# Kernel tuning notes

Hardware: AMD Instinct MI355X
Metric: run time of the kernel (lower is better)

Reference implementation:

```python
import jax, jax.numpy as jnp
import numpy as np

B, T, QD, KD, AD = 64, 2048, 512, 512, 512
SCALING = 1.0
NEG = -1e10


def setup_inputs() -> dict:
    key = jax.random.key(0)
    ks = jax.random.split(key, 10)
    s = 0.02
    return {
        "query": jax.random.normal(ks[0], (B, QD), jnp.float32),
        "keys": jax.random.normal(ks[1], (B, T, KD), jnp.float32),
        "value": jax.random.normal(ks[2], (B, T, KD), jnp.float32),
        "cover": jax.random.uniform(ks[3], (B, T), jnp.float32),
        "key_len": jax.random.randint(ks[4], (B,), T // 2, T + 1),
        "Wq": jax.random.normal(ks[5], (QD, AD), jnp.float32) * s,
        "bq": jnp.zeros((AD,), jnp.float32),
        "Wk": jax.random.normal(ks[6], (KD, AD), jnp.float32) * s,
        "Wc": jax.random.normal(ks[7], (1, AD), jnp.float32) * s,
        "Wo": jax.random.normal(ks[8], (AD, 1), jnp.float32) * s,
    }


def reference(query, keys, value, cover, key_len, Wq, bq, Wk, Wc, Wo):
    # projections
    q = query @ Wq + bq                      # [B, A]
    k = jnp.einsum("btd,da->bta", keys, Wk)  # [B, T, A]
    c = cover[..., None] * Wc[0]             # [B, T, A]  (Linear(1, A), no bias)
    # additive energy
    e = jnp.tanh(q[:, None, :] + k + c)      # [B, T, A]
    energy = jnp.einsum("bta,ao->bot", e, Wo)  # [B, 1, T]
    # mask padded positions (t >= key_len)
    mask = jnp.arange(T)[None, None, :] >= key_len[:, None, None]  # [B, 1, T]
    energy = jnp.where(mask, NEG, energy)
    attn = jax.nn.softmax(energy * SCALING, axis=2)  # [B, 1, T]
    context = jnp.einsum("bqt,btd->bqd", attn, value)[:, 0, :]  # [B, KD]
    return context, attn
```

## Files before the change

### kernel.cpp

```cpp
#include <hip/hip_runtime.h>
#include <hip/hip_bf16.h>

#define B_ 64
#define T_ 2048
#define D_ 512
#define A_ 512
#define BM 128
#define BN 128
#define BK 32
#define NSTEP (D_/BK)

typedef float f32x4_t __attribute__((ext_vector_type(4)));
typedef short bf16x8_t __attribute__((ext_vector_type(8)));

#define GLL16(g, l) __builtin_amdgcn_global_load_lds( \
    (const __attribute__((address_space(1))) void*)(g), \
    (__attribute__((address_space(3))) void*)(l), 16, 0, 0)

__device__ __forceinline__ uint2 pack8u(float4 v0, float4 v1) {
  union { __hip_bfloat162 h[2]; uint2 u; } r;
  r.h[0] = __float22bfloat162_rn(make_float2(v0.x, v0.y));
  r.h[1] = __float22bfloat162_rn(make_float2(v0.z, v0.w));
  uint2 lo = r.u;
  r.h[0] = __float22bfloat162_rn(make_float2(v1.x, v1.y));
  r.h[1] = __float22bfloat162_rn(make_float2(v1.z, v1.w));
  return make_uint2(lo.x, lo.y), r.u;
}

__global__ void __launch_bounds__(256) qproj_kernel(
    const float* __restrict__ query, const float* __restrict__ Wq,
    const float* __restrict__ bq, float* __restrict__ qbuf) {
  __shared__ float qs[D_];
  const int b = blockIdx.x, tid = threadIdx.x;
  qs[tid] = query[b*D_ + tid];
  qs[tid+256] = query[b*D_ + tid + 256];
  __syncthreads();
  float a0 = bq[tid], a1 = bq[tid+256];
  for (int d = 0; d < D_; ++d) {
    const float qv = qs[d];
    a0 += qv * Wq[d*A_ + tid];
    a1 += qv * Wq[d*A_ + tid + 256];
  }
  qbuf[b*A_ + tid] = a0;
  qbuf[b*A_ + tid+256] = a1;
}

__global__ void __launch_bounds__(256) wkprep_kernel(
    const float* __restrict__ Wk, unsigned int* __restrict__ slab) {
  __shared__ float tile[32][65];
  const int kb = blockIdx.x >> 3;
  const int a0 = (blockIdx.x & 7) * 64;
  const int tid = threadIdx.x;
  for (int p = 0; p < 8; ++p) {
    const int idx = p*256 + tid;
    const int k = idx >> 6, al = idx & 63;
    tile[k][al] = Wk[(kb*32 + k)*A_ + a0 + al];
  }
  __syncthreads();
  const int al = tid >> 2, c = tid & 3;
  const int a = a0 + al;
  union { __hip_bfloat162 h[2]; uint2 u; } w0, w1;
  w0.h[0] = __float22bfloat162_rn(make_float2(tile[c*8+0][al], tile[c*8+1][al]));
  w0.h[1] = __float22bfloat162_rn(make_float2(tile[c*8+2][al], tile[c*8+3][al]));
  w1.h[0] = __float22bfloat162_rn(make_float2(tile[c*8+4][al], tile[c*8+5][al]));
  w1.h[1] = __float22bfloat162_rn(make_float2(tile[c*8+6][al], tile[c*8+7][al]));
  const int cpos = c ^ ((a >> 1) & 3);
  *(uint4*)(slab + (kb*512 + a)*16 + cpos*4) =
      make_uint4(w0.u.x, w0.u.y, w1.u.x, w1.u.y);
}

__global__ void __launch_bounds__(256, 4) energy_kernel(
    const float* __restrict__ keys, const float* __restrict__ cover,
    const int* __restrict__ key_len, const unsigned char* __restrict__ slab,
    const float* __restrict__ qbuf, const float* __restrict__ Wc,
    const float* __restrict__ Wo, float* __restrict__ epart) {
  __shared__ __align__(16) unsigned char Abuf[2][BM*64];
  __shared__ __align__(16) unsigned char Bbuf[2][BN*64];
  __shared__ float redbuf[4][64];

  const int d = blockIdx.x;
  const int logical = (d & 7) * 512 + (d >> 3);
  const int ct = logical & 3;
  const int tt = (logical >> 2) & 15;
  const int b  = logical >> 6;

  const int t0 = tt * BM;
  const int kl = key_len[b];
  if (t0 >= kl) return;

  const int tid = threadIdx.x;
  const int wid = tid >> 6;
  const int lane = tid & 63;
  const int lq = lane >> 4, lr = lane & 15;
  const int wm = wid >> 1, wn = wid & 1;

  const int arow = tid >> 1, ahalf = tid & 1;
  const float* aptr = keys + ((size_t)b * T_ + t0 + arow) * D_ + ahalf * 16;
  const int as = (arow >> 1) & 3;
  const int ad0 = arow*64 + (((ahalf*2+0) ^ as) << 4);
  const int ad1 = arow*64 + (((ahalf*2+1) ^ as) << 4);

  const unsigned char* bsl = slab + ct * 8192 + wid * 1024 + lane * 16;

  f32x4_t acc[4][4];
  #pragma unroll
  for (int i = 0; i < 4; ++i)
    #pragma unroll
    for (int j = 0; j < 4; ++j) acc[i][j] = 0.0f;

  int a_off[4], b_off[4];
  #pragma unroll
  for (int mf = 0; mf < 4; ++mf) {
    const int r = wm*64 + mf*16 + lr;
    a_off[mf] = r*64 + ((lq ^ ((r >> 1) & 3)) << 4);
  }
  #pragma unroll
  for (int nf = 0; nf < 4; ++nf) {
    const int r = wn*64 + nf*16 + lr;
    b_off[nf] = r*64 + ((lq ^ ((r >> 1) & 3)) << 4);
  }

  {
    const float4 v0 = *(const float4*)(aptr);
    const float4 v1 = *(const float4*)(aptr + 4);
    const float4 v2 = *(const float4*)(aptr + 8);
    const float4 v3 = *(const float4*)(aptr + 12);
    union { __hip_bfloat162 h[2]; uint2 u; } p0, p1, p2, p3;
    p0.h[0] = __float22bfloat162_rn(make_float2(v0.x, v0.y));
    p0.h[1] = __float22bfloat162_rn(make_float2(v0.z, v0.w));
    p1.h[0] = __float22bfloat162_rn(make_float2(v1.x, v1.y));
    p1.h[1] = __float22bfloat162_rn(make_float2(v1.z, v1.w));
    p2.h[0] = __float22bfloat162_rn(make_float2(v2.x, v2.y));
    p2.h[1] = __float22bfloat162_rn(make_float2(v2.z, v2.w));
    p3.h[0] = __float22bfloat162_rn(make_float2(v3.x, v3.y));
    p3.h[1] = __float22bfloat162_rn(make_float2(v3.z, v3.w));
    *(uint4*)(&Abuf[0][ad0]) = make_uint4(p0.u.x, p0.u.y, p1.u.x, p1.u.y);
    *(uint4*)(&Abuf[0][ad1]) = make_uint4(p2.u.x, p2.u.y, p3.u.x, p3.u.y);
    GLL16(bsl,        &Bbuf[0][wid*1024]);
    GLL16(bsl + 4096, &Bbuf[0][4096 + wid*1024]);
  }
  __syncthreads();

  for (int ks = 0; ks < NSTEP; ++ks) {
    const int cur = ks & 1;
    const bool pre = (ks + 1 < NSTEP);
    float4 v0, v1, v2, v3;
    if (pre) {
      const float* p = aptr + (ks + 1) * BK;
      v0 = *(const float4*)(p);
      v1 = *(const float4*)(p + 4);
      v2 = *(const float4*)(p + 8);
      v3 = *(const float4*)(p + 12);
      const unsigned char* g = bsl + (size_t)(ks+1)*32768;
      GLL16(g,        &Bbuf[cur^1][wid*1024]);
      GLL16(g + 4096, &Bbuf[cur^1][4096 + wid*1024]);
    }
    bf16x8_t aF[4], bF[4];
    #pragma unroll
    for (int mf = 0; mf < 4; ++mf) aF[mf] = *(const bf16x8_t*)(&Abuf[cur][a_off[mf]]);
    #pragma unroll
    for (int nf = 0; nf < 4; ++nf) bF[nf] = *(const bf16x8_t*)(&Bbuf[cur][b_off[nf]]);
    #pragma unroll
    for (int mf = 0; mf < 4; ++mf)
      #pragma unroll
      for (int nf = 0; nf < 4; ++nf)
        acc[mf][nf] = __builtin_amdgcn_mfma_f32_16x16x32_bf16(aF[mf], bF[nf], acc[mf][nf], 0, 0, 0);
    if (pre) {
      union { __hip_bfloat162 h[2]; uint2 u; } p0, p1, p2, p3;
      p0.h[0] = __float22bfloat162_rn(make_float2(v0.x, v0.y));
      p0.h[1] = __float22bfloat162_rn(make_float2(v0.z, v0.w));
      p1.h[0] = __float22bfloat162_rn(make_float2(v1.x, v1.y));
      p1.h[1] = __float22bfloat162_rn(make_float2(v1.z, v1.w));
      p2.h[0] = __float22bfloat162_rn(make_float2(v2.x, v2.y));
      p2.h[1] = __float22bfloat162_rn(make_float2(v2.z, v2.w));
      p3.h[0] = __float22bfloat162_rn(make_float2(v3.x, v3.y));
      p3.h[1] = __float22bfloat162_rn(make_float2(v3.z, v3.w));
      *(uint4*)(&Abuf[cur^1][ad0]) = make_uint4(p0.u.x, p0.u.y, p1.u.x, p1.u.y);
      *(uint4*)(&Abuf[cur^1][ad1]) = make_uint4(p2.u.x, p2.u.y, p3.u.x, p3.u.y);
    }
    __syncthreads();
  }

  float cov[4][4];
  #pragma unroll
  for (int mf = 0; mf < 4; ++mf)
    #pragma unroll
    for (int j = 0; j < 4; ++j)
      cov[mf][j] = cover[(size_t)b*T_ + t0 + wm*64 + mf*16 + lq*4 + j];

  float ep[4][4];
  #pragma unroll
  for (int mf = 0; mf < 4; ++mf)
    #pragma unroll
    for (int j = 0; j < 4; ++j) ep[mf][j] = 0.f;

  #pragma unroll
  for (int nf = 0; nf < 4; ++nf) {
    const int n = ct*BN + wn*64 + nf*16 + lr;
    const float qv = qbuf[b*A_ + n];
    const float wc = Wc[n];
    const float wo = Wo[n];
    #pragma unroll
    for (int mf = 0; mf < 4; ++mf)
      #pragma unroll
      for (int j = 0; j < 4; ++j) {
        float p = acc[mf][nf][j] + qv + cov[mf][j] * wc;
        p = fminf(fmaxf(p, -15.f), 15.f);
        const float t2 = __expf(2.f * p);
        ep[mf][j] += wo * ((t2 - 1.f) * __builtin_amdgcn_rcpf(t2 + 1.f));
      }
  }
  #pragma unroll
  for (int mf = 0; mf < 4; ++mf)
    #pragma unroll
    for (int j = 0; j < 4; ++j) {
      float v = ep[mf][j];
      v += __shfl_xor(v, 1); v += __shfl_xor(v, 2);
      v += __shfl_xor(v, 4); v += __shfl_xor(v, 8);
      ep[mf][j] = v;
    }
  if (lr == 0) {
    #pragma unroll
    for (int mf = 0; mf < 4; ++mf)
      #pragma unroll
      for (int j = 0; j < 4; ++j)
        redbuf[wid][mf*16 + lq*4 + j] = ep[mf][j];
  }
  __syncthreads();
  if (tid < BM) {
    const int wmm = tid >> 6, rl = tid & 63;
    epart[((size_t)ct*B_ + b)*T_ + t0 + tid] = redbuf[wmm*2][rl] + redbuf[wmm*2+1][rl];
  }
}

__global__ void __launch_bounds__(1024) softmax_kernel(
    const float* __restrict__ epart, const int* __restrict__ key_len,
    float* __restrict__ attn) {
  __shared__ float sredM[16];
  __shared__ float sredS[16];
  const int b = blockIdx.x, tid = threadIdx.x;
  const int kl = key_len[b];
  float e0 = -3.0e38f, e1 = -3.0e38f;
  if (tid < kl)
    e0 = epart[(size_t)b*T_ + tid] + epart[((size_t)B_ + b)*T_ + tid]
       + epart[((size_t)2*B_ + b)*T_ + tid] + epart[((size_t)3*B_ + b)*T_ + tid];
  if (tid + 1024 < kl)
    e1 = epart[(size_t)b*T_ + tid+1024] + epart[((size_t)B_ + b)*T_ + tid+1024]
       + epart[((size_t)2*B_ + b)*T_ + tid+1024] + epart[((size_t)3*B_ + b)*T_ + tid+1024];
  float m = fmaxf(e0, e1);
  for (int s = 32; s; s >>= 1) m = fmaxf(m, __shfl_xor(m, s));
  if ((tid & 63) == 0) sredM[tid >> 6] = m;
  __syncthreads();
  float M = -3.0e38f;
  #pragma unroll
  for (int i = 0; i < 16; ++i) M = fmaxf(M, sredM[i]);
  const float p0 = (tid < kl) ? __expf(e0 - M) : 0.f;
  const float p1 = (tid + 1024 < kl) ? __expf(e1 - M) : 0.f;
  float s = p0 + p1;
  for (int k = 32; k; k >>= 1) s += __shfl_xor(s, k);
  if ((tid & 63) == 0) sredS[tid >> 6] = s;
  __syncthreads();
  float S = 0.f;
  #pragma unroll
  for (int i = 0; i < 16; ++i) S += sredS[i];
  const float inv = 1.f / S;
  attn[b*T_ + tid] = p0 * inv;
  attn[b*T_ + tid + 1024] = p1 * inv;
}

__global__ void __launch_bounds__(256) ctxpart_kernel(
    const float* __restrict__ value, const float* __restrict__ attn,
    const int* __restrict__ key_len, float* __restrict__ partial) {
  __shared__ float att_s[256];
  const int b = blockIdx.y, ch = blockIdx.x;
  const int tid = threadIdx.x;
  const int kl = key_len[b];
  const int tstart = ch * 256;
  const int tend = min(256, kl - tstart);
  float ax = 0.f, ay = 0.f;
  if (tend > 0) {
    att_s[tid] = attn[b*T_ + tstart + tid];
    __syncthreads();
    const float2* vp = (const float2*)(value + ((size_t)b*T_ + tstart)*D_) + tid;
    #pragma unroll 4
    for (int i = 0; i < tend; ++i) {
      const float w = att_s[i];
      const float2 v = vp[(size_t)i * 256];
      ax += w * v.x; ay += w * v.y;
    }
  }
  float2* pp = (float2*)(partial + (size_t)(b*8 + ch)*D_) + tid;
  *pp = make_float2(ax, ay);
}

__global__ void __launch_bounds__(256) ctxsum_kernel(
    const float* __restrict__ partial, float* __restrict__ ctx) {
  const int b = blockIdx.x, tid = threadIdx.x;
  float sx = 0.f, sy = 0.f;
  #pragma unroll
  for (int c = 0; c < 8; ++c) {
    const float2 v = *((const float2*)(partial + (size_t)(b*8 + c)*D_) + tid);
    sx += v.x; sy += v.y;
  }
  *((float2*)(ctx + (size_t)b*D_) + tid) = make_float2(sx, sy);
}

extern "C" void kernel_launch(void* const* d_in, const int* in_sizes, int n_in,
                              void* d_out, int out_size, void* d_ws, size_t ws_size,
                              hipStream_t stream) {
  const float* query  = (const float*)d_in[0];
  const float* keys   = (const float*)d_in[1];
  const float* value  = (const float*)d_in[2];
  const float* cover  = (const float*)d_in[3];
  const int*   key_len= (const int*)d_in[4];
  const float* Wq     = (const float*)d_in[5];
  const float* bq     = (const float*)d_in[6];
  const float* Wk     = (const float*)d_in[7];
  const float* Wc     = (const float*)d_in[8];
  const float* Wo     = (const float*)d_in[9];

  float* out = (float*)d_out;
  float* ctx_out  = out;
  float* attn_out = out + B_*A_;

  float* ws = (float*)d_ws;
  float* qbuf    = ws;
  float* epart   = ws + 32768;
  float* partial = ws + 32768 + 524288;
  unsigned int* slab = (unsigned int*)(ws + 32768 + 524288 + 262144);

  qproj_kernel<<<B_, 256, 0, stream>>>(query, Wq, bq, qbuf);
  wkprep_kernel<<<128, 256, 0, stream>>>(Wk, slab);
  energy_kernel<<<B_*(T_/BM)*(A_/BN), 256, 0, stream>>>(
      keys, cover, key_len, (const unsigned char*)slab, qbuf, Wc, Wo, epart);
  softmax_kernel<<<B_, 1024, 0, stream>>>(epart, key_len, attn_out);
  ctxpart_kernel<<<dim3(8, B_), 256, 0, stream>>>(value, attn_out, key_len, partial);
  ctxsum_kernel<<<B_, 256, 0, stream>>>(partial, ctx_out);
}
```

Baseline: 224.6 us.

## Stream fp32 keys into LDS via global_load_lds and convert to bf16 at fragment load

The keys tile is now copied asynchronously into shared memory as fp32 with direct global-to-LDS loads, using an XOR-swizzled layout, instead of being loaded into registers and converted to bf16 before the LDS store. The bf16 conversion moves to the point where each wave reads its MFMA A fragments. This frees registers and takes the conversion and LDS store off the prefetch path, but it doubles the LDS footprint for A and makes every wave convert redundantly. Launch bounds occupancy is lowered from 4 to 3 to match.

```diff
diff --git a/kernel.cpp b/kernel.cpp
--- a/kernel.cpp
+++ b/kernel.cpp
@@ -16,16 +16,6 @@
 #define GLL16(g, l) __builtin_amdgcn_global_load_lds( \
     (const __attribute__((address_space(1))) void*)(g), \
     (__attribute__((address_space(3))) void*)(l), 16, 0, 0)
-
-__device__ __forceinline__ uint2 pack8u(float4 v0, float4 v1) {
-  union { __hip_bfloat162 h[2]; uint2 u; } r;
-  r.h[0] = __float22bfloat162_rn(make_float2(v0.x, v0.y));
-  r.h[1] = __float22bfloat162_rn(make_float2(v0.z, v0.w));
-  uint2 lo = r.u;
-  r.h[0] = __float22bfloat162_rn(make_float2(v1.x, v1.y));
-  r.h[1] = __float22bfloat162_rn(make_float2(v1.z, v1.w));
-  return make_uint2(lo.x, lo.y), r.u;
-}
 
 __global__ void __launch_bounds__(256) qproj_kernel(
     const float* __restrict__ query, const float* __restrict__ Wq,
@@ -69,12 +59,12 @@
       make_uint4(w0.u.x, w0.u.y, w1.u.x, w1.u.y);
 }
 
-__global__ void __launch_bounds__(256, 4) energy_kernel(
+__global__ void __launch_bounds__(256, 3) energy_kernel(
     const float* __restrict__ keys, const float* __restrict__ cover,
     const int* __restrict__ key_len, const unsigned char* __restrict__ slab,
     const float* __restrict__ qbuf, const float* __restrict__ Wc,
     const float* __restrict__ Wo, float* __restrict__ epart) {
-  __shared__ __align__(16) unsigned char Abuf[2][BM*64];
+  __shared__ __align__(16) float Afp[2][BM*BK];
   __shared__ __align__(16) unsigned char Bbuf[2][BN*64];
   __shared__ float redbuf[4][64];
 
@@ -94,12 +84,14 @@
   const int lq = lane >> 4, lr = lane & 15;
   const int wm = wid >> 1, wn = wid & 1;
 
-  const int arow = tid >> 1, ahalf = tid & 1;
-  const float* aptr = keys + ((size_t)b * T_ + t0 + arow) * D_ + ahalf * 16;
-  const int as = (arow >> 1) & 3;
-  const int ad0 = arow*64 + (((ahalf*2+0) ^ as) << 4);
-  const int ad1 = arow*64 + (((ahalf*2+1) ^ as) << 4);
-
+  const int lrow = lane >> 3;
+  const int lchunk = (lane & 7) ^ lrow;
+  const float* agA[4];
+  #pragma unroll
+  for (int j = 0; j < 4; ++j) {
+    const int r = (wid*4 + j)*8 + lrow;
+    agA[j] = keys + ((size_t)b * T_ + t0 + r) * D_ + lchunk * 4;
+  }
   const unsigned char* bsl = slab + ct * 8192 + wid * 1024 + lane * 16;
 
   f32x4_t acc[4][4];
@@ -108,34 +100,24 @@
     #pragma unroll
     for (int j = 0; j < 4; ++j) acc[i][j] = 0.0f;
 
-  int a_off[4], b_off[4];
-  #pragma unroll
-  for (int mf = 0; mf < 4; ++mf) {
-    const int r = wm*64 + mf*16 + lr;
-    a_off[mf] = r*64 + ((lq ^ ((r >> 1) & 3)) << 4);
-  }
+  int b_off[4];
   #pragma unroll
   for (int nf = 0; nf < 4; ++nf) {
     const int r = wn*64 + nf*16 + lr;
     b_off[nf] = r*64 + ((lq ^ ((r >> 1) & 3)) << 4);
   }
+  int a_off0[4], a_off1[4];
+  #pragma unroll
+  for (int mf = 0; mf < 4; ++mf) {
+    const int r = wm*64 + mf*16 + lr;
+    a_off0[mf] = r*BK + (((lq*2 + 0) ^ (r & 7)) << 2);
+    a_off1[mf] = r*BK + (((lq*2 + 1) ^ (r & 7)) << 2);
+  }
 
   {
-    const float4 v0 = *(const float4*)(aptr);
-    const float4 v1 = *(const float4*)(aptr + 4);
-    const float4 v2 = *(const float4*)(aptr + 8);
-    const float4 v3 = *(const float4*)(aptr + 12);
-    union { __hip_bfloat162 h[2]; uint2 u; } p0, p1, p2, p3;
-    p0.h[0] = __float22bfloat162_rn(make_float2(v0.x, v0.y));
-    p0.h[1] = __float22bfloat162_rn(make_float2(v0.z, v0.w));
-    p1.h[0] = __float22bfloat162_rn(make_float2(v1.x, v1.y));
-    p1.h[1] = __float22bfloat162_rn(make_float2(v1.z, v1.w));
-    p2.h[0] = __float22bfloat162_rn(make_float2(v2.x, v2.y));
-    p2.h[1] = __float22bfloat162_rn(make_float2(v2.z, v2.w));
-    p3.h[0] = __float22bfloat162_rn(make_float2(v3.x, v3.y));
-    p3.h[1] = __float22bfloat162_rn(make_float2(v3.z, v3.w));
-    *(uint4*)(&Abuf[0][ad0]) = make_uint4(p0.u.x, p0.u.y, p1.u.x, p1.u.y);
-    *(uint4*)(&Abuf[0][ad1]) = make_uint4(p2.u.x, p2.u.y, p3.u.x, p3.u.y);
+    #pragma unroll
+    for (int j = 0; j < 4; ++j)
+      GLL16(agA[j], &Afp[0][(wid*4 + j)*256]);
     GLL16(bsl,        &Bbuf[0][wid*1024]);
     GLL16(bsl + 4096, &Bbuf[0][4096 + wid*1024]);
   }
@@ -143,21 +125,26 @@
 
   for (int ks = 0; ks < NSTEP; ++ks) {
     const int cur = ks & 1;
-    const bool pre = (ks + 1 < NSTEP);
-    float4 v0, v1, v2, v3;
-    if (pre) {
-      const float* p = aptr + (ks + 1) * BK;
-      v0 = *(const float4*)(p);
-      v1 = *(const float4*)(p + 4);
-      v2 = *(const float4*)(p + 8);
-      v3 = *(const float4*)(p + 12);
+    if (ks + 1 < NSTEP) {
+      #pragma unroll
+      for (int j = 0; j < 4; ++j)
+        GLL16(agA[j] + (ks+1)*BK, &Afp[cur^1][(wid*4 + j)*256]);
       const unsigned char* g = bsl + (size_t)(ks+1)*32768;
       GLL16(g,        &Bbuf[cur^1][wid*1024]);
       GLL16(g + 4096, &Bbuf[cur^1][4096 + wid*1024]);
     }
     bf16x8_t aF[4], bF[4];
     #pragma unroll
-    for (int mf = 0; mf < 4; ++mf) aF[mf] = *(const bf16x8_t*)(&Abuf[cur][a_off[mf]]);
+    for (int mf = 0; mf < 4; ++mf) {
+      const f32x4_t lo = *(const f32x4_t*)(&Afp[cur][a_off0[mf]]);
+      const f32x4_t hi = *(const f32x4_t*)(&Afp[cur][a_off1[mf]]);
+      union { __hip_bfloat162 h[4]; bf16x8_t v; } pk;
+      pk.h[0] = __float22bfloat162_rn(make_float2(lo[0], lo[1]));
+      pk.h[1] = __float22bfloat162_rn(make_float2(lo[2], lo[3]));
+      pk.h[2] = __float22bfloat162_rn(make_float2(hi[0], hi[1]));
+      pk.h[3] = __float22bfloat162_rn(make_float2(hi[2], hi[3]));
+      aF[mf] = pk.v;
+    }
     #pragma unroll
     for (int nf = 0; nf < 4; ++nf) bF[nf] = *(const bf16x8_t*)(&Bbuf[cur][b_off[nf]]);
     #pragma unroll
@@ -165,19 +152,6 @@
       #pragma unroll
       for (int nf = 0; nf < 4; ++nf)
         acc[mf][nf] = __builtin_amdgcn_mfma_f32_16x16x32_bf16(aF[mf], bF[nf], acc[mf][nf], 0, 0, 0);
-    if (pre) {
-      union { __hip_bfloat162 h[2]; uint2 u; } p0, p1, p2, p3;
-      p0.h[0] = __float22bfloat162_rn(make_float2(v0.x, v0.y));
-      p0.h[1] = __float22bfloat162_rn(make_float2(v0.z, v0.w));
-      p1.h[0] = __float22bfloat162_rn(make_float2(v1.x, v1.y));
-      p1.h[1] = __float22bfloat162_rn(make_float2(v1.z, v1.w));
-      p2.h[0] = __float22bfloat162_rn(make_float2(v2.x, v2.y));
-      p2.h[1] = __float22bfloat162_rn(make_float2(v2.z, v2.w));
-      p3.h[0] = __float22bfloat162_rn(make_float2(v3.x, v3.y));
-      p3.h[1] = __float22bfloat162_rn(make_float2(v3.z, v3.w));
-      *(uint4*)(&Abuf[cur^1][ad0]) = make_uint4(p0.u.x, p0.u.y, p1.u.x, p1.u.y);
-      *(uint4*)(&Abuf[cur^1][ad1]) = make_uint4(p2.u.x, p2.u.y, p3.u.x, p3.u.y);
-    }
     __syncthreads();
   }
 
```

New measurement: 233.4 us. 4.0% more time.
